# Kernel tuning notes

Hardware: AMD Instinct MI355X
Metric: run time of the kernel (lower is better)

The kernel has to match this reference:

```python
import jax, jax.numpy as jnp
import numpy as np

N, P, Q, T, J, B, H = 262144, 64, 64, 2048, 512, 8, 64


def setup_inputs() -> dict:
    key = jax.random.key(0)
    ks = jax.random.split(key, 11)
    sH = 1.0 / np.sqrt(H).astype(np.float32)
    return {
        "idx": jax.random.randint(ks[0], (B,), 0, J),
        "seg_ids": jnp.sort(jax.random.randint(ks[1], (N,), 0, T)),
        "K": jax.random.normal(ks[2], (N, P), jnp.float32) * 0.1,
        "V": jax.random.normal(ks[3], (N, Q), jnp.float32),
        "S": jax.random.normal(ks[4], (P, J), jnp.float32) * 0.1,
        "W_ih": jax.random.normal(ks[5], (3 * H, Q), jnp.float32) * sH,
        "W_hh": jax.random.normal(ks[6], (3 * H, H), jnp.float32) * sH,
        "b_ih": jax.random.normal(ks[7], (3 * H,), jnp.float32) * sH,
        "b_hh": jax.random.normal(ks[8], (3 * H,), jnp.float32) * sH,
        "w_out": jax.random.normal(ks[9], (1, H), jnp.float32) * sH,
        "b_out": jax.random.normal(ks[10], (1,), jnp.float32) * sH,
    }


def reference(idx, seg_ids, K, V, S, W_ih, W_hh, b_ih, b_hh, w_out, b_out):
    # W[:, b] = K @ S[:, idx[b]]  -> [N, B]
    w = K @ S[:, idx]
    # ragged per-segment softmax over the N axis (segments = date windows)
    m = jax.ops.segment_max(w, seg_ids, num_segments=T)          # [T, B]
    e = jnp.exp(w - m[seg_ids])                                  # [N, B]
    denom = jax.ops.segment_sum(e, seg_ids, num_segments=T)     # [T, B]
    alpha = e / denom[seg_ids]                                   # [N, B]
    # weighted aggregation of V rows per segment: M[t, b] = sum_u alpha_u * V_u
    M = jax.ops.segment_sum(alpha[:, :, None] * V[:, None, :],
                            seg_ids, num_segments=T)             # [T, B, Q]
    X = jnp.transpose(M, (1, 0, 2))                              # [B, T, Q]

    # PyTorch GRU (gate order r,z,n). Faithful to the original bug: GRU was
    # built without batch_first=True, so axis 0 (B) is time, axis 1 (T) is batch.
    def step(h, x_t):  # x_t: [T, Q], h: [T, H]
        gi = x_t @ W_ih.T + b_ih                                 # [T, 3H]
        gh = h @ W_hh.T + b_hh                                   # [T, 3H]
        i_r, i_z, i_n = jnp.split(gi, 3, axis=1)
        h_r, h_z, h_n = jnp.split(gh, 3, axis=1)
        r = jax.nn.sigmoid(i_r + h_r)
        z = jax.nn.sigmoid(i_z + h_z)
        n = jnp.tanh(i_n + r * h_n)
        h_new = (1.0 - z) * n + z * h
        return h_new, h_new

    h0 = jnp.zeros((T, H), X.dtype)
    _, hs = jax.lax.scan(step, h0, X)                            # [B, T, H]
    preds = hs @ w_out.T + b_out                                 # [B, T, 1]
    return preds
```

## Files before the change

kernel.cpp:

```cpp
#include <hip/hip_runtime.h>
#include <math.h>

#define NN 262144
#define PP 64
#define QQ 64
#define TT 2048
#define JJ 512
#define BB 8
#define HH 64

__device__ __forceinline__ float lane_bcast(float v, int l) {
  return __int_as_float(__builtin_amdgcn_readlane(__float_as_int(v), l));
}

__global__ void k_prep(const int* __restrict__ seg_ids, const int* __restrict__ idx,
                       const float* __restrict__ S, int* __restrict__ seg_start,
                       float* __restrict__ s_cols) {
  int tid = blockIdx.x * blockDim.x + threadIdx.x;
  if (tid <= TT) {
    int lo = 0, hi = NN;
    while (lo < hi) {
      int mid = (lo + hi) >> 1;
      int v = seg_ids[mid];
      if (v < tid) lo = mid + 1; else hi = mid;
    }
    seg_start[tid] = lo;
  }
  int t2 = tid - (TT + 1);
  if (t2 >= 0 && t2 < PP * BB) {
    int p = t2 >> 3, b = t2 & 7;
    s_cols[b * PP + p] = S[p * JJ + idx[b]];
  }
}

__global__ __launch_bounds__(256) void k_w(const float* __restrict__ Kmat,
                                           const float* __restrict__ s_cols,
                                           float* __restrict__ ew) {
  __shared__ __align__(16) float s_lds[BB * PP];
  int tid = threadIdx.x;
  for (int i = tid; i < BB * PP; i += 256) s_lds[i] = s_cols[i];
  __syncthreads();
  int n = blockIdx.x * 64 + (tid >> 2);
  int sub = tid & 3;
  const float4* Kp = reinterpret_cast<const float4*>(Kmat + (size_t)n * PP + sub * 16);
  float4 kq[4];
#pragma unroll
  for (int j = 0; j < 4; ++j) kq[j] = Kp[j];
  float acc[8];
#pragma unroll
  for (int b = 0; b < 8; ++b) acc[b] = 0.f;
#pragma unroll
  for (int j4 = 0; j4 < 4; ++j4) {
    float4 kk = kq[j4];
#pragma unroll
    for (int b = 0; b < 8; ++b) {
      const float4 sv = *reinterpret_cast<const float4*>(&s_lds[b * PP + sub * 16 + j4 * 4]);
      acc[b] += kk.x * sv.x + kk.y * sv.y + kk.z * sv.z + kk.w * sv.w;
    }
  }
#pragma unroll
  for (int b = 0; b < 8; ++b) {
    acc[b] += __shfl_xor(acc[b], 1);
    acc[b] += __shfl_xor(acc[b], 2);
  }
  float ox = (sub == 0) ? acc[0] : (sub == 1) ? acc[2] : (sub == 2) ? acc[4] : acc[6];
  float oy = (sub == 0) ? acc[1] : (sub == 1) ? acc[3] : (sub == 2) ? acc[5] : acc[7];
  reinterpret_cast<float2*>(ew + (size_t)n * 8)[sub] =
      make_float2(__expf(ox), __expf(oy));
}

__global__ __launch_bounds__(256) void k_seg(const float* __restrict__ ew,
                                             const float* __restrict__ V,
                                             const int* __restrict__ seg_start,
                                             float* __restrict__ M) {
  __shared__ __align__(16) float alpha[128 * 8];
  __shared__ float accred[4][8][64];
  __shared__ float reds[4][8];
  __shared__ float bcast[8];
  int t = blockIdx.x;
  int s = seg_start[t], e = seg_start[t + 1];
  int tid = threadIdx.x;
  int lane = tid & 63, wv = tid >> 6;
  int rsub = lane >> 4;
  int qg = lane & 15;

  float se = 0.f;
  float4 acc[8];
#pragma unroll
  for (int b = 0; b < 8; ++b) acc[b] = make_float4(0.f, 0.f, 0.f, 0.f);

  for (int base = s; base < e; base += 128) {
    int cnt = e - base; if (cnt > 128) cnt = 128;
    __syncthreads();
    for (int i = tid; i < cnt * 8; i += 256) {
      float ev = ew[(size_t)base * 8 + i];
      alpha[i] = ev;
      se += ev;
    }
    __syncthreads();
#pragma unroll
    for (int i = 0; i < 8; ++i) {
      int r = wv * 32 + i * 4 + rsub;
      if (r < cnt) {
        float4 vv = reinterpret_cast<const float4*>(V + (size_t)(base + r) * QQ)[qg];
        const float4* al = reinterpret_cast<const float4*>(&alpha[r * 8]);
        float4 a0 = al[0], a1 = al[1];
        acc[0].x += a0.x * vv.x; acc[0].y += a0.x * vv.y; acc[0].z += a0.x * vv.z; acc[0].w += a0.x * vv.w;
        acc[1].x += a0.y * vv.x; acc[1].y += a0.y * vv.y; acc[1].z += a0.y * vv.z; acc[1].w += a0.y * vv.w;
        acc[2].x += a0.z * vv.x; acc[2].y += a0.z * vv.y; acc[2].z += a0.z * vv.z; acc[2].w += a0.z * vv.w;
        acc[3].x += a0.w * vv.x; acc[3].y += a0.w * vv.y; acc[3].z += a0.w * vv.z; acc[3].w += a0.w * vv.w;
        acc[4].x += a1.x * vv.x; acc[4].y += a1.x * vv.y; acc[4].z += a1.x * vv.z; acc[4].w += a1.x * vv.w;
        acc[5].x += a1.y * vv.x; acc[5].y += a1.y * vv.y; acc[5].z += a1.y * vv.z; acc[5].w += a1.y * vv.w;
        acc[6].x += a1.z * vv.x; acc[6].y += a1.z * vv.y; acc[6].z += a1.z * vv.z; acc[6].w += a1.z * vv.w;
        acc[7].x += a1.w * vv.x; acc[7].y += a1.w * vv.y; acc[7].z += a1.w * vv.z; acc[7].w += a1.w * vv.w;
      }
    }
  }

#pragma unroll
  for (int b = 0; b < 8; ++b) {
    acc[b].x += __shfl_xor(acc[b].x, 16); acc[b].y += __shfl_xor(acc[b].y, 16);
    acc[b].z += __shfl_xor(acc[b].z, 16); acc[b].w += __shfl_xor(acc[b].w, 16);
    acc[b].x += __shfl_xor(acc[b].x, 32); acc[b].y += __shfl_xor(acc[b].y, 32);
    acc[b].z += __shfl_xor(acc[b].z, 32); acc[b].w += __shfl_xor(acc[b].w, 32);
  }

  se += __shfl_xor(se, 8);
  se += __shfl_xor(se, 16);
  se += __shfl_xor(se, 32);
  __syncthreads();
  if (lane < 8) reds[wv][lane] = se;
  if (rsub == 0) {
#pragma unroll
    for (int b = 0; b < 8; ++b)
      *reinterpret_cast<float4*>(&accred[wv][b][qg * 4]) = acc[b];
  }
  __syncthreads();
  if (tid < 8) {
    float dd = reds[0][tid] + reds[1][tid] + reds[2][tid] + reds[3][tid];
    bcast[tid] = (dd > 0.f) ? 1.f / dd : 0.f;
  }
  __syncthreads();
  for (int o = tid; o < 512; o += 256) {
    int b = o >> 6, q = o & 63;
    float sum = accred[0][b][q] + accred[1][b][q] + accred[2][b][q] + accred[3][b][q];
    M[(size_t)t * 512 + o] = sum * bcast[b];
  }
}

__global__ __launch_bounds__(256) void k_gi(const float* __restrict__ M,
                                            const float* __restrict__ W_ih,
                                            const float* __restrict__ b_ih,
                                            float* __restrict__ GI) {
  __shared__ float Wt[64 * 193];
  int tid = threadIdx.x;
  for (int i = tid; i < 192 * 64; i += 256) {
    int g = i >> 6, k = i & 63;
    Wt[k * 193 + g] = W_ih[i];
  }
  __syncthreads();
  int lane = tid & 63, wv = tid >> 6;
  int row0 = blockIdx.x * 32 + wv * 8;
  float x[8];
#pragma unroll
  for (int rr = 0; rr < 8; ++rr) {
    int rho = row0 + rr;
    int b = rho >> 11, t = rho & 2047;
    x[rr] = M[((size_t)t * 8 + b) * 64 + lane];
  }
  float bi0 = b_ih[lane], bi1 = b_ih[64 + lane], bi2 = b_ih[128 + lane];
  float a0[8], a1[8], a2[8];
#pragma unroll
  for (int rr = 0; rr < 8; ++rr) { a0[rr] = bi0; a1[rr] = bi1; a2[rr] = bi2; }
#pragma unroll
  for (int k = 0; k < 64; ++k) {
    float w0 = Wt[k * 193 + lane];
    float w1 = Wt[k * 193 + 64 + lane];
    float w2 = Wt[k * 193 + 128 + lane];
#pragma unroll
    for (int rr = 0; rr < 8; ++rr) {
      float xk = lane_bcast(x[rr], k);
      a0[rr] += w0 * xk; a1[rr] += w1 * xk; a2[rr] += w2 * xk;
    }
  }
#pragma unroll
  for (int rr = 0; rr < 8; ++rr) {
    size_t rho = (size_t)row0 + rr;
    GI[rho * 192 + lane]       = a0[rr];
    GI[rho * 192 + 64 + lane]  = a1[rr];
    GI[rho * 192 + 128 + lane] = a2[rr];
  }
}

__global__ __launch_bounds__(256) void k_gru(const float* __restrict__ GI,
                                             const float* __restrict__ W_hh,
                                             const float* __restrict__ b_hh,
                                             const float* __restrict__ w_out,
                                             const float* __restrict__ b_out,
                                             float* __restrict__ preds) {
  __shared__ float Wt[64 * 193];
  int tid = threadIdx.x;
  for (int i = tid; i < 192 * 64; i += 256) {
    int g = i >> 6, k = i & 63;
    Wt[k * 193 + g] = W_hh[i];
  }
  __syncthreads();
  int lane = tid & 63, wv = tid >> 6;
  int t = blockIdx.x * 4 + wv;
  float bh0 = b_hh[lane], bh1 = b_hh[64 + lane], bh2 = b_hh[128 + lane];
  float wo = w_out[lane];
  float bo = b_out[0];

  float gr[8], gz[8], gn[8];
#pragma unroll
  for (int b = 0; b < 8; ++b) {
    size_t base = ((size_t)b * TT + t) * 192;
    gr[b] = GI[base + lane];
    gz[b] = GI[base + 64 + lane];
    gn[b] = GI[base + 128 + lane];
  }

  float h;
  {
    float r = 1.f / (1.f + __expf(-(gr[0] + bh0)));
    float z = 1.f / (1.f + __expf(-(gz[0] + bh1)));
    float nv = tanhf(gn[0] + r * bh2);
    h = (1.f - z) * nv;
    float pv = h * wo;
#pragma unroll
    for (int off = 32; off; off >>= 1) pv += __shfl_xor(pv, off);
    if (lane == 0) preds[t] = pv + bo;
  }
#pragma unroll
  for (int b = 1; b < 8; ++b) {
    float ar = bh0, az = bh1, an = bh2;
#pragma unroll
    for (int k = 0; k < 64; ++k) {
      float hk = lane_bcast(h, k);
      float w0 = Wt[k * 193 + lane];
      float w1 = Wt[k * 193 + 64 + lane];
      float w2 = Wt[k * 193 + 128 + lane];
      ar += w0 * hk; az += w1 * hk; an += w2 * hk;
    }
    float r = 1.f / (1.f + __expf(-(gr[b] + ar)));
    float z = 1.f / (1.f + __expf(-(gz[b] + az)));
    float nv = tanhf(gn[b] + r * an);
    h = (1.f - z) * nv + z * h;
    float pv = h * wo;
#pragma unroll
    for (int off = 32; off; off >>= 1) pv += __shfl_xor(pv, off);
    if (lane == 0) preds[(size_t)b * TT + t] = pv + bo;
  }
}

extern "C" void kernel_launch(void* const* d_in, const int* in_sizes, int n_in,
                              void* d_out, int out_size, void* d_ws, size_t ws_size,
                              hipStream_t stream) {
  const int*   idx     = (const int*)d_in[0];
  const int*   seg_ids = (const int*)d_in[1];
  const float* Kmat    = (const float*)d_in[2];
  const float* V       = (const float*)d_in[3];
  const float* S       = (const float*)d_in[4];
  const float* W_ih    = (const float*)d_in[5];
  const float* W_hh    = (const float*)d_in[6];
  const float* b_ih    = (const float*)d_in[7];
  const float* b_hh    = (const float*)d_in[8];
  const float* w_out   = (const float*)d_in[9];
  const float* b_out   = (const float*)d_in[10];
  float* out = (float*)d_out;

  char* ws = (char*)d_ws;
  int*   seg_start = (int*)(ws + 0);
  float* s_cols    = (float*)(ws + 8448);
  float* ew        = (float*)(ws + 10496);
  float* M         = (float*)(ws + 8399104);
  float* GI        = (float*)(ws + 12593408);

  hipLaunchKernelGGL(k_prep, dim3(11), dim3(256), 0, stream, seg_ids, idx, S, seg_start, s_cols);
  hipLaunchKernelGGL(k_w, dim3(NN / 64), dim3(256), 0, stream, Kmat, s_cols, ew);
  hipLaunchKernelGGL(k_seg, dim3(TT), dim3(256), 0, stream, ew, V, seg_start, M);
  hipLaunchKernelGGL(k_gi, dim3(512), dim3(256), 0, stream, M, W_ih, b_ih, GI);
  hipLaunchKernelGGL(k_gru, dim3(512), dim3(256), 0, stream, GI, W_hh, b_hh, w_out, b_out, out);
}
```

Baseline: 79.70 us.

## Process one segment per wavefront in k_seg, removing shared-memory staging and block syncs

The segment aggregation kernel now gives each wavefront its own segment (4 segments per block) instead of one segment per 256-thread block. The exp weights are read straight from global memory as float4 pairs, and both the denominators and the weighted V sums are reduced with lane shuffles. This drops the LDS staging, the cross-wave reduction and all __syncthreads. The cost is less parallelism per segment (about 128 rows serially per wave) and load imbalance between segments of different sizes within a block.

```diff
diff --git a/kernel.cpp b/kernel.cpp
--- a/kernel.cpp
+++ b/kernel.cpp
@@ -73,47 +73,35 @@
                                              const float* __restrict__ V,
                                              const int* __restrict__ seg_start,
                                              float* __restrict__ M) {
-  __shared__ __align__(16) float alpha[128 * 8];
-  __shared__ float accred[4][8][64];
-  __shared__ float reds[4][8];
-  __shared__ float bcast[8];
-  int t = blockIdx.x;
+  int lane = threadIdx.x & 63, wv = threadIdx.x >> 6;
+  int t = blockIdx.x * 4 + wv;
   int s = seg_start[t], e = seg_start[t + 1];
-  int tid = threadIdx.x;
-  int lane = tid & 63, wv = tid >> 6;
   int rsub = lane >> 4;
   int qg = lane & 15;
 
-  float se = 0.f;
   float4 acc[8];
 #pragma unroll
   for (int b = 0; b < 8; ++b) acc[b] = make_float4(0.f, 0.f, 0.f, 0.f);
-
-  for (int base = s; base < e; base += 128) {
-    int cnt = e - base; if (cnt > 128) cnt = 128;
-    __syncthreads();
-    for (int i = tid; i < cnt * 8; i += 256) {
-      float ev = ew[(size_t)base * 8 + i];
-      alpha[i] = ev;
-      se += ev;
-    }
-    __syncthreads();
-#pragma unroll
-    for (int i = 0; i < 8; ++i) {
-      int r = wv * 32 + i * 4 + rsub;
-      if (r < cnt) {
-        float4 vv = reinterpret_cast<const float4*>(V + (size_t)(base + r) * QQ)[qg];
-        const float4* al = reinterpret_cast<const float4*>(&alpha[r * 8]);
-        float4 a0 = al[0], a1 = al[1];
-        acc[0].x += a0.x * vv.x; acc[0].y += a0.x * vv.y; acc[0].z += a0.x * vv.z; acc[0].w += a0.x * vv.w;
-        acc[1].x += a0.y * vv.x; acc[1].y += a0.y * vv.y; acc[1].z += a0.y * vv.z; acc[1].w += a0.y * vv.w;
-        acc[2].x += a0.z * vv.x; acc[2].y += a0.z * vv.y; acc[2].z += a0.z * vv.z; acc[2].w += a0.z * vv.w;
-        acc[3].x += a0.w * vv.x; acc[3].y += a0.w * vv.y; acc[3].z += a0.w * vv.z; acc[3].w += a0.w * vv.w;
-        acc[4].x += a1.x * vv.x; acc[4].y += a1.x * vv.y; acc[4].z += a1.x * vv.z; acc[4].w += a1.x * vv.w;
-        acc[5].x += a1.y * vv.x; acc[5].y += a1.y * vv.y; acc[5].z += a1.y * vv.z; acc[5].w += a1.y * vv.w;
-        acc[6].x += a1.z * vv.x; acc[6].y += a1.z * vv.y; acc[6].z += a1.z * vv.z; acc[6].w += a1.z * vv.w;
-        acc[7].x += a1.w * vv.x; acc[7].y += a1.w * vv.y; acc[7].z += a1.w * vv.z; acc[7].w += a1.w * vv.w;
-      }
+  float4 selo = make_float4(0.f, 0.f, 0.f, 0.f);
+  float4 sehi = make_float4(0.f, 0.f, 0.f, 0.f);
+
+  int nq = (e - s + 3) >> 2;
+  for (int i = 0; i < nq; ++i) {
+    int r = s + i * 4 + rsub;
+    if (r < e) {
+      const float4* ewp = reinterpret_cast<const float4*>(ew + (size_t)r * 8);
+      float4 elo = ewp[0], ehi = ewp[1];
+      float4 vv = reinterpret_cast<const float4*>(V + (size_t)r * QQ)[qg];
+      selo.x += elo.x; selo.y += elo.y; selo.z += elo.z; selo.w += elo.w;
+      sehi.x += ehi.x; sehi.y += ehi.y; sehi.z += ehi.z; sehi.w += ehi.w;
+      acc[0].x += elo.x * vv.x; acc[0].y += elo.x * vv.y; acc[0].z += elo.x * vv.z; acc[0].w += elo.x * vv.w;
+      acc[1].x += elo.y * vv.x; acc[1].y += elo.y * vv.y; acc[1].z += elo.y * vv.z; acc[1].w += elo.y * vv.w;
+      acc[2].x += elo.z * vv.x; acc[2].y += elo.z * vv.y; acc[2].z += elo.z * vv.z; acc[2].w += elo.z * vv.w;
+      acc[3].x += elo.w * vv.x; acc[3].y += elo.w * vv.y; acc[3].z += elo.w * vv.z; acc[3].w += elo.w * vv.w;
+      acc[4].x += ehi.x * vv.x; acc[4].y += ehi.x * vv.y; acc[4].z += ehi.x * vv.z; acc[4].w += ehi.x * vv.w;
+      acc[5].x += ehi.y * vv.x; acc[5].y += ehi.y * vv.y; acc[5].z += ehi.y * vv.z; acc[5].w += ehi.y * vv.w;
+      acc[6].x += ehi.z * vv.x; acc[6].y += ehi.z * vv.y; acc[6].z += ehi.z * vv.z; acc[6].w += ehi.z * vv.w;
+      acc[7].x += ehi.w * vv.x; acc[7].y += ehi.w * vv.y; acc[7].z += ehi.w * vv.z; acc[7].w += ehi.w * vv.w;
     }
   }
 
@@ -124,27 +112,31 @@
     acc[b].x += __shfl_xor(acc[b].x, 32); acc[b].y += __shfl_xor(acc[b].y, 32);
     acc[b].z += __shfl_xor(acc[b].z, 32); acc[b].w += __shfl_xor(acc[b].w, 32);
   }
-
-  se += __shfl_xor(se, 8);
-  se += __shfl_xor(se, 16);
-  se += __shfl_xor(se, 32);
-  __syncthreads();
-  if (lane < 8) reds[wv][lane] = se;
+  selo.x += __shfl_xor(selo.x, 16); selo.y += __shfl_xor(selo.y, 16);
+  selo.z += __shfl_xor(selo.z, 16); selo.w += __shfl_xor(selo.w, 16);
+  sehi.x += __shfl_xor(sehi.x, 16); sehi.y += __shfl_xor(sehi.y, 16);
+  sehi.z += __shfl_xor(sehi.z, 16); sehi.w += __shfl_xor(sehi.w, 16);
+  selo.x += __shfl_xor(selo.x, 32); selo.y += __shfl_xor(selo.y, 32);
+  selo.z += __shfl_xor(selo.z, 32); selo.w += __shfl_xor(selo.w, 32);
+  sehi.x += __shfl_xor(sehi.x, 32); sehi.y += __shfl_xor(sehi.y, 32);
+  sehi.z += __shfl_xor(sehi.z, 32); sehi.w += __shfl_xor(sehi.w, 32);
+
   if (rsub == 0) {
-#pragma unroll
-    for (int b = 0; b < 8; ++b)
-      *reinterpret_cast<float4*>(&accred[wv][b][qg * 4]) = acc[b];
-  }
-  __syncthreads();
-  if (tid < 8) {
-    float dd = reds[0][tid] + reds[1][tid] + reds[2][tid] + reds[3][tid];
-    bcast[tid] = (dd > 0.f) ? 1.f / dd : 0.f;
-  }
-  __syncthreads();
-  for (int o = tid; o < 512; o += 256) {
-    int b = o >> 6, q = o & 63;
-    float sum = accred[0][b][q] + accred[1][b][q] + accred[2][b][q] + accred[3][b][q];
-    M[(size_t)t * 512 + o] = sum * bcast[b];
+    float inv[8];
+    inv[0] = (selo.x > 0.f) ? 1.f / selo.x : 0.f;
+    inv[1] = (selo.y > 0.f) ? 1.f / selo.y : 0.f;
+    inv[2] = (selo.z > 0.f) ? 1.f / selo.z : 0.f;
+    inv[3] = (selo.w > 0.f) ? 1.f / selo.w : 0.f;
+    inv[4] = (sehi.x > 0.f) ? 1.f / sehi.x : 0.f;
+    inv[5] = (sehi.y > 0.f) ? 1.f / sehi.y : 0.f;
+    inv[6] = (sehi.z > 0.f) ? 1.f / sehi.z : 0.f;
+    inv[7] = (sehi.w > 0.f) ? 1.f / sehi.w : 0.f;
+#pragma unroll
+    for (int b = 0; b < 8; ++b) {
+      float4 o = make_float4(acc[b].x * inv[b], acc[b].y * inv[b],
+                             acc[b].z * inv[b], acc[b].w * inv[b]);
+      *reinterpret_cast<float4*>(M + (size_t)t * 512 + b * 64 + qg * 4) = o;
+    }
   }
 }
 
@@ -278,7 +270,7 @@
 
   hipLaunchKernelGGL(k_prep, dim3(11), dim3(256), 0, stream, seg_ids, idx, S, seg_start, s_cols);
   hipLaunchKernelGGL(k_w, dim3(NN / 64), dim3(256), 0, stream, Kmat, s_cols, ew);
-  hipLaunchKernelGGL(k_seg, dim3(TT), dim3(256), 0, stream, ew, V, seg_start, M);
+  hipLaunchKernelGGL(k_seg, dim3(TT / 4), dim3(256), 0, stream, ew, V, seg_start, M);
   hipLaunchKernelGGL(k_gi, dim3(512), dim3(256), 0, stream, M, W_ih, b_ih, GI);
   hipLaunchKernelGGL(k_gru, dim3(512), dim3(256), 0, stream, GI, W_hh, b_hh, w_out, b_out, out);
 }
```

Measured after the change: 80.54 us. No clear change (+1.1%).
